# Performance work log

Hardware: AMD Instinct MI355X
Metric: run time of the kernel (lower is better)

## Reference

```python
import jax, jax.numpy as jnp
import numpy as np

B, T, N = 16, 256, 20000
REGIONS, TOPK = 20000, 0.2
IN_DIM = int(REGIONS * TOPK ** 2)   # 800
K = int(REGIONS * TOPK)             # 4000
R = 1000                            # rest_limitation
ZCOLS = K + R                       # all-False mask columns per sample


def setup_inputs() -> dict:
    key = jax.random.key(0)
    ks = jax.random.split(key, 8)
    x = jax.random.normal(ks[0], (B, T, IN_DIM), jnp.float32)
    # first ZCOLS voxel columns are never covered (mask False), rest are covered
    border_mask = jnp.concatenate(
        [jnp.zeros((B, T, ZCOLS), bool), jnp.ones((B, T, N - ZCOLS), bool)], axis=-1)
    # K distinct indices per sample, drawn from the uncovered columns [0, ZCOLS)
    index = jax.vmap(lambda k: jax.random.permutation(k, ZCOLS)[:K])(
        jax.random.split(ks[1], B)).astype(jnp.int32)
    s1 = 1.0 / np.sqrt(IN_DIM); s2 = 1.0 / np.sqrt(K)
    W1 = jax.random.uniform(ks[2], (IN_DIM, K), jnp.float32, -s1, s1)
    b1 = jax.random.uniform(ks[3], (K,), jnp.float32, -s1, s1)
    W2 = jax.random.uniform(ks[4], (K, K), jnp.float32, -s2, s2)
    b2 = jax.random.uniform(ks[5], (K,), jnp.float32, -s2, s2)
    W3 = jax.random.uniform(ks[6], (K, R), jnp.float32, -s2, s2)
    b3 = jax.random.uniform(ks[7], (R,), jnp.float32, -s2, s2)
    return dict(x=x, border_mask=border_mask, index=index,
                W1=W1, b1=b1, W2=W2, b2=b2, W3=W3, b3=b3)


def reference(x, border_mask, index, W1, b1, W2, b2, W3, b3):
    h = x @ W1 + b1                  # unzip   [B,T,K]
    h = h @ W2 + b2                  # unprocess [B,T,K]
    x_rest = h @ W3 + b3             # rest    [B,T,R]
    colsum = border_mask.sum(axis=1)                 # [B,N] per-voxel coverage count
    idx_member = jax.vmap(lambda i: jnp.zeros((N,), bool).at[i].set(True))(index)
    # scatter h into indexed voxel columns
    x_recon = jax.vmap(lambda i, hb: jnp.zeros((T, N), h.dtype).at[:, i].set(hb))(index, h)
    # rest positions: uncovered columns not already taken by index (sorted order)
    rest_mask = (colsum == 0) & ~idx_member          # [B,N]
    rank = jnp.cumsum(rest_mask, axis=-1) - 1        # position among rest columns
    valid = rest_mask & (rank < R)                   # cap at rest_limitation ('adjust')
    g = jnp.take_along_axis(
        x_rest, jnp.broadcast_to(jnp.clip(rank, 0, R - 1)[:, None, :], (B, T, N)), axis=-1)
    return jnp.where(valid[:, None, :], g, x_recon)
```

## Files before the change

### kernel.cpp

```cpp
#include <hip/hip_runtime.h>

typedef __attribute__((ext_vector_type(4))) float f32x4;
typedef __attribute__((ext_vector_type(8))) __bf16 bf16x8;

#define B_SZ   16
#define T_SZ   256
#define BT_SZ  4096
#define N_VOX  20000
#define INDIM  800
#define K1P    1024
#define K_DIM  4000
#define KP     4096
#define R_DIM  1000
#define RP     1024

__device__ __forceinline__ unsigned short f2bf(float f) {
  unsigned int u = __builtin_bit_cast(unsigned int, f);
  u += 0x7fffu + ((u >> 16) & 1u);
  return (unsigned short)(u >> 16);
}
__device__ __forceinline__ float bf2f(unsigned short h) {
  unsigned int u = ((unsigned int)h) << 16;
  return __builtin_bit_cast(float, u);
}
__device__ __forceinline__ void gload16(const void* g, void* l) {
  __builtin_amdgcn_global_load_lds(
      (const __attribute__((address_space(1))) void*)g,
      (__attribute__((address_space(3))) void*)l, 16, 0, 0);
}

__global__ void cvt_pad_x(const float* __restrict__ src,
                          unsigned short* __restrict__ dst) {
  int i = blockIdx.x * 256 + threadIdx.x;
  int row = i >> 8;
  int c4 = i & 255;
  if (row >= BT_SZ) return;
  ushort4 o = {0, 0, 0, 0};
  if (c4 < INDIM / 4) {
    float4 v = ((const float4*)(src + (size_t)row * INDIM))[c4];
    o.x = f2bf(v.x); o.y = f2bf(v.y); o.z = f2bf(v.z); o.w = f2bf(v.w);
  }
  ((ushort4*)(dst + (size_t)row * K1P))[c4] = o;
}

__global__ void transpose_cvt(const float* __restrict__ W,
                              unsigned short* __restrict__ WT,
                              int K, int N, int Kpad, int Npad) {
  __shared__ float tile[32][33];
  int k0 = blockIdx.x * 32, n0 = blockIdx.y * 32;
  for (int i = threadIdx.y; i < 32; i += 8) {
    int k = k0 + i, n = n0 + threadIdx.x;
    tile[i][threadIdx.x] = (k < K && n < N) ? W[(size_t)k * N + n] : 0.f;
  }
  __syncthreads();
  for (int i = threadIdx.y; i < 32; i += 8) {
    int n = n0 + i, k = k0 + threadIdx.x;
    if (n < Npad && k < Kpad)
      WT[(size_t)n * Kpad + k] = f2bf(tile[threadIdx.x][i]);
  }
}

__global__ void covered_kernel(const int* __restrict__ bmask,
                               unsigned char* __restrict__ cov) {
  int n4 = blockIdx.x * 256 + threadIdx.x;
  int b = blockIdx.y;
  if (n4 >= N_VOX / 4) return;
  const int4* p = (const int4*)(bmask + (size_t)b * T_SZ * N_VOX) + n4;
  int4 a = {0, 0, 0, 0};
  for (int t0 = 0; t0 < T_SZ; t0 += 8) {
    int4 c[8];
#pragma unroll
    for (int tt = 0; tt < 8; ++tt)
      c[tt] = p[(size_t)(t0 + tt) * (N_VOX / 4)];
#pragma unroll
    for (int tt = 0; tt < 8; ++tt) {
      a.x |= c[tt].x; a.y |= c[tt].y; a.z |= c[tt].z; a.w |= c[tt].w;
    }
    if (a.x && a.y && a.z && a.w) break;
  }
  uchar4 o;
  o.x = (unsigned char)(a.x != 0); o.y = (unsigned char)(a.y != 0);
  o.z = (unsigned char)(a.z != 0); o.w = (unsigned char)(a.w != 0);
  *(uchar4*)(cov + (size_t)b * N_VOX + (size_t)n4 * 4) = o;
}

__global__ void map_kernel(const int* __restrict__ index,
                           const unsigned char* __restrict__ cov,
                           int* __restrict__ srcmap) {
  int b = blockIdx.x, tid = threadIdx.x;
  int* sm = srcmap + (size_t)b * N_VOX;
  for (int n = tid; n < N_VOX; n += 1024) sm[n] = -1;
  __syncthreads();
  const int* idx = index + (size_t)b * K_DIM;
  for (int j = tid; j < K_DIM; j += 1024) sm[idx[j]] = j;
  __syncthreads();

  __shared__ int wsum[16];
  __shared__ int s_running;
  if (tid == 0) s_running = 0;
  __syncthreads();
  const int lane = tid & 63, wid = tid >> 6;
  const unsigned char* cv = cov + (size_t)b * N_VOX;
  for (int base = 0; base < N_VOX; base += 1024) {
    int n = base + tid;
    bool flag = (n < N_VOX) && (!cv[n]) && (sm[n] < 0);
    unsigned long long bal = __ballot(flag);
    if (lane == 0) wsum[wid] = __popcll(bal);
    __syncthreads();
    int woff = 0, tot = 0;
    for (int w = 0; w < 16; ++w) {
      int c = wsum[w];
      if (w < wid) woff += c;
      tot += c;
    }
    int rank = s_running + woff + __popcll(bal & ((1ull << lane) - 1ull));
    if (flag && rank < R_DIM) sm[n] = K_DIM + rank;
    __syncthreads();
    if (tid == 0) s_running += tot;
    __syncthreads();
  }
}

template <int BM>
__global__ __launch_bounds__(256) void gemm_bt(
    const unsigned short* __restrict__ A,
    const unsigned short* __restrict__ BTm,
    const float* __restrict__ bias, int nbias,
    unsigned short* __restrict__ C,
    int K, int lda, int ldb, int ldc) {
  constexpr int MI = BM / 32;
  __shared__ __align__(16) unsigned short As[BM * 32];
  __shared__ __align__(16) unsigned short Bs[128 * 32];
  const int tid = threadIdx.x;
  const int wid = tid >> 6;
  const int lane = tid & 63;
  const int bm = blockIdx.y, bn = blockIdx.x;
  const int wm = wid >> 1, wn = wid & 1;
  const int sub = lane >> 2;
  const int quad = lane & 3;

  const int rA0 = wid * 16 + sub;
  const char* gA0 = (const char*)(A + (size_t)(bm * BM + rA0) * lda) + quad * 16;
  const char* gA1 = (const char*)(A + (size_t)(bm * BM + ((BM == 128) ? rA0 + 64 : rA0)) * lda) + quad * 16;
  const char* gB0 = (const char*)(BTm + (size_t)(bn * 128 + rA0) * ldb) + quad * 16;
  const char* gB1 = (const char*)(BTm + (size_t)(bn * 128 + rA0 + 64) * ldb) + quad * 16;

  char* lA0 = (char*)As + wid * 1024 + lane * 16;
  char* lA1 = lA0 + 4096;
  char* lB0 = (char*)Bs + wid * 1024 + lane * 16;
  char* lB1 = lB0 + 4096;

  const int r15 = lane & 15;
  const int kg = lane >> 4;

  f32x4 acc[MI][4] = {};

  for (int kt = 0; kt < K; kt += 32) {
    const int kb = kt * 2;
    gload16(gA0 + kb, lA0);
    if constexpr (BM == 128) gload16(gA1 + kb, lA1);
    gload16(gB0 + kb, lB0);
    gload16(gB1 + kb, lB1);
    __syncthreads();
    bf16x8 af[MI], bfr[4];
#pragma unroll
    for (int i = 0; i < MI; ++i)
      af[i] = *(const bf16x8*)&As[(wm * (BM / 2) + i * 16 + r15) * 32 + kg * 8];
#pragma unroll
    for (int j = 0; j < 4; ++j)
      bfr[j] = *(const bf16x8*)&Bs[(wn * 64 + j * 16 + r15) * 32 + kg * 8];
#pragma unroll
    for (int i = 0; i < MI; ++i)
#pragma unroll
      for (int j = 0; j < 4; ++j)
        acc[i][j] = __builtin_amdgcn_mfma_f32_16x16x32_bf16(af[i], bfr[j], acc[i][j], 0, 0, 0);
    __syncthreads();
  }

#pragma unroll
  for (int i = 0; i < MI; ++i) {
    const int row0 = bm * BM + wm * (BM / 2) + i * 16 + kg * 4;
#pragma unroll
    for (int j = 0; j < 4; ++j) {
      const int col = bn * 128 + wn * 64 + j * 16 + r15;
      const float bv = bias[(col < nbias) ? col : (nbias - 1)];
#pragma unroll
      for (int r = 0; r < 4; ++r)
        C[(size_t)(row0 + r) * ldc + col] = f2bf(acc[i][j][r] + bv);
    }
  }
}

__global__ __launch_bounds__(512, 2) void gemm256(
    const unsigned short* __restrict__ A,
    const unsigned short* __restrict__ BTm,
    const float* __restrict__ bias, int nbias,
    unsigned short* __restrict__ C,
    int K, int lda, int ldb, int ldc) {
  __shared__ __align__(16) char smem[131072];
  const int tid = threadIdx.x;
  const int wid = tid >> 6, lane = tid & 63;
  const int wm = wid >> 2, wn = wid & 3;
  const int r15 = lane & 15, kg = lane >> 4;
  const int bm = blockIdx.y, bn = blockIdx.x;

  const int srow = tid >> 2;
  const int scol = (tid & 3) * 8;
  const unsigned short* gA = A + (size_t)(bm * 256 + srow) * lda + scol;
  const unsigned short* gB = BTm + (size_t)(bn * 256 + srow) * ldb + scol;

  const int aoff = (wm * 128 + r15) * 64 + kg * 16;
  const int boff = (wn * 64 + r15) * 64 + kg * 16;

  f32x4 acc[8][4] = {};
  bf16x8 bfr[4];

#define STAGE_HALF(S, MAT, KH, TN)                                            \
  {                                                                           \
    const unsigned short* g =                                                 \
        ((MAT) ? gB : gA) + (size_t)(TN) * 64 + (KH) * 32;                    \
    char* l = smem + (S) * 65536 + (MAT) * 32768 + (KH) * 16384 + tid * 16;   \
    gload16(g, l);                                                            \
    gload16(g + (size_t)128 * ((MAT) ? ldb : lda), l + 8192);                 \
  }

#define PHASE(S, KS, MH, TN, DOVM)                                            \
  {                                                                           \
    bf16x8 af[4];                                                             \
    if ((MH) == 0) {                                                          \
      _Pragma("unroll")                                                       \
      for (int j = 0; j < 4; ++j)                                             \
        bfr[j] = *(const bf16x8*)(smem + (S) * 65536 + 32768 +                \
                                  (KS) * 16384 + boff + j * 1024);            \
    }                                                                         \
    _Pragma("unroll")                                                         \
    for (int i = 0; i < 4; ++i)                                               \
      af[i] = *(const bf16x8*)(smem + (S) * 65536 + (KS) * 16384 +            \
                               (MH) * 4096 + aoff + i * 1024);                \
    STAGE_HALF((S) ^ 1, (MH), (KS), TN)                                       \
    if (DOVM) asm volatile("s_waitcnt vmcnt(4)" ::: "memory");                \
    asm volatile("s_barrier" ::: "memory");                                   \
    __builtin_amdgcn_s_setprio(1);                                            \
    _Pragma("unroll")                                                         \
    for (int i = 0; i < 4; ++i)                                               \
      _Pragma("unroll")                                                       \
      for (int j = 0; j < 4; ++j)                                             \
        acc[(MH) * 4 + i][j] = __builtin_amdgcn_mfma_f32_16x16x32_bf16(       \
            af[i], bfr[j], acc[(MH) * 4 + i][j], 0, 0, 0);                    \
    __builtin_amdgcn_s_setprio(0);                                            \
    asm volatile("s_barrier" ::: "memory");                                   \
  }

#define TILE4(S, TN)                                                          \
  PHASE(S, 0, 0, TN, 0)                                                       \
  PHASE(S, 0, 1, TN, 1)                                                       \
  PHASE(S, 1, 0, TN, 0)                                                       \
  PHASE(S, 1, 1, TN, 1)

  const int NT = K >> 6;
  STAGE_HALF(0, 0, 0, 0)
  STAGE_HALF(0, 1, 0, 0)
  STAGE_HALF(0, 0, 1, 0)
  STAGE_HALF(0, 1, 1, 0)
  asm volatile("s_waitcnt vmcnt(4)" ::: "memory");
  asm volatile("s_barrier" ::: "memory");

  for (int tp = 0; tp < NT; tp += 2) {
    const int tn1 = tp + 1;
    TILE4(0, tn1)
    const int tn2 = (tp + 2 < NT) ? tp + 2 : NT - 1;
    TILE4(1, tn2)
  }

#undef STAGE_HALF
#undef PHASE
#undef TILE4

#pragma unroll
  for (int f = 0; f < 8; ++f) {
    const int row0 = bm * 256 + wm * 128 + f * 16 + kg * 4;
#pragma unroll
    for (int j = 0; j < 4; ++j) {
      const int col = bn * 256 + wn * 64 + j * 16 + r15;
      const float bv = bias[(col < nbias) ? col : (nbias - 1)];
#pragma unroll
      for (int r = 0; r < 4; ++r)
        C[(size_t)(row0 + r) * ldc + col] = f2bf(acc[f][j][r] + bv);
    }
  }
}

__global__ void fill_out(const int* __restrict__ srcmap,
                         const unsigned short* __restrict__ h2b,
                         const unsigned short* __restrict__ xrb,
                         float* __restrict__ out) {
  int n4 = blockIdx.x * 256 + threadIdx.x;
  if (n4 >= N_VOX / 4) return;
  int t = blockIdx.y, b = blockIdx.z;
  size_t bt = (size_t)b * T_SZ + t;
  const int4 sm = ((const int4*)(srcmap + (size_t)b * N_VOX))[n4];
  const unsigned short* hrow = h2b + bt * KP;
  const unsigned short* xrow = xrb + bt * RP;
  float4 v;
  v.x = (sm.x < 0) ? 0.f : bf2f(sm.x < K_DIM ? hrow[sm.x] : xrow[sm.x - K_DIM]);
  v.y = (sm.y < 0) ? 0.f : bf2f(sm.y < K_DIM ? hrow[sm.y] : xrow[sm.y - K_DIM]);
  v.z = (sm.z < 0) ? 0.f : bf2f(sm.z < K_DIM ? hrow[sm.z] : xrow[sm.z - K_DIM]);
  v.w = (sm.w < 0) ? 0.f : bf2f(sm.w < K_DIM ? hrow[sm.w] : xrow[sm.w - K_DIM]);
  ((float4*)(out + bt * N_VOX))[n4] = v;
}

extern "C" void kernel_launch(void* const* d_in, const int* in_sizes, int n_in,
                              void* d_out, int out_size, void* d_ws, size_t ws_size,
                              hipStream_t stream) {
  const float* x          = (const float*)d_in[0];
  const int* bm           = (const int*)d_in[1];
  const int* index        = (const int*)d_in[2];
  const float* W1         = (const float*)d_in[3];
  const float* b1         = (const float*)d_in[4];
  const float* W2         = (const float*)d_in[5];
  const float* b2         = (const float*)d_in[6];
  const float* W3         = (const float*)d_in[7];
  const float* b3         = (const float*)d_in[8];
  float* out = (float*)d_out;

  char* ws = (char*)d_ws;
  size_t off = 0;
  auto alloc = [&](size_t bytes) -> void* {
    void* p = ws + off;
    off += (bytes + 255) & ~(size_t)255;
    return p;
  };
  unsigned short* xb  = (unsigned short*)alloc((size_t)BT_SZ * K1P * 2);
  unsigned short* w1t = (unsigned short*)alloc((size_t)KP * K1P * 2);
  unsigned short* w2t = (unsigned short*)alloc((size_t)KP * KP * 2);
  unsigned short* w3t = (unsigned short*)alloc((size_t)RP * KP * 2);
  unsigned short* h1b = (unsigned short*)alloc((size_t)BT_SZ * KP * 2);
  unsigned short* h2b = (unsigned short*)alloc((size_t)BT_SZ * KP * 2);
  unsigned short* xrb = (unsigned short*)alloc((size_t)BT_SZ * RP * 2);
  unsigned char* cov = (unsigned char*)alloc((size_t)B_SZ * N_VOX);
  int* srcmap = (int*)alloc((size_t)B_SZ * N_VOX * 4);

  cvt_pad_x<<<BT_SZ * (K1P / 4) / 256, 256, 0, stream>>>(x, xb);
  {
    dim3 g(K1P / 32, KP / 32);
    transpose_cvt<<<g, dim3(32, 8), 0, stream>>>(W1, w1t, INDIM, K_DIM, K1P, KP);
  }
  {
    dim3 g(KP / 32, KP / 32);
    transpose_cvt<<<g, dim3(32, 8), 0, stream>>>(W2, w2t, K_DIM, K_DIM, KP, KP);
  }
  {
    dim3 g(KP / 32, RP / 32);
    transpose_cvt<<<g, dim3(32, 8), 0, stream>>>(W3, w3t, K_DIM, R_DIM, KP, RP);
  }

  {
    dim3 g((N_VOX / 4 + 255) / 256, B_SZ);
    covered_kernel<<<g, 256, 0, stream>>>(bm, cov);
  }
  map_kernel<<<B_SZ, 1024, 0, stream>>>(index, cov, srcmap);

  {
    dim3 g(KP / 256, BT_SZ / 256);
    gemm256<<<g, 512, 0, stream>>>(xb, w1t, b1, K_DIM, h1b, K1P, K1P, K1P, KP);
  }
  {
    dim3 g(KP / 256, BT_SZ / 256);
    gemm256<<<g, 512, 0, stream>>>(h1b, w2t, b2, K_DIM, h2b, KP, KP, KP, KP);
  }
  {
    dim3 g(RP / 128, BT_SZ / 64);
    gemm_bt<64><<<g, 256, 0, stream>>>(h2b, w3t, b3, R_DIM, xrb, KP, KP, KP, RP);
  }

  {
    dim3 g((N_VOX / 4 + 255) / 256, T_SZ, B_SZ);
    fill_out<<<g, 256, 0, stream>>>(srcmap, h2b, xrb, out);
  }
}
```

Measured before the change: 487.8 us.

## Split-K third GEMM, swizzle LDS in gemm256, trim K padding, nontemporal output stores

The third GEMM now uses 128-row tiles with a 4-way K split that writes bf16 partials, followed by a new reduce kernel that adds the bias. The first GEMM's K padding shrinks from 1024 to 896, cutting wasted MFMA work. gemm256 gains an XOR swizzle on LDS writes and reads to avoid bank conflicts, and fill_out uses nontemporal stores for the large output. Rounding each split-K partial to bf16 adds extra rounding error and extra memory traffic. The 896 pad must also divide cleanly into gemm256's K stepping.

```diff
diff --git a/kernel.cpp b/kernel.cpp
--- a/kernel.cpp
+++ b/kernel.cpp
@@ -8,11 +8,12 @@
 #define BT_SZ  4096
 #define N_VOX  20000
 #define INDIM  800
-#define K1P    1024
+#define K1P    896
 #define K_DIM  4000
 #define KP     4096
 #define R_DIM  1000
 #define RP     1024
+#define SPLITK 4
 
 __device__ __forceinline__ unsigned short f2bf(float f) {
   unsigned int u = __builtin_bit_cast(unsigned int, f);
@@ -31,10 +32,9 @@
 
 __global__ void cvt_pad_x(const float* __restrict__ src,
                           unsigned short* __restrict__ dst) {
-  int i = blockIdx.x * 256 + threadIdx.x;
-  int row = i >> 8;
-  int c4 = i & 255;
-  if (row >= BT_SZ) return;
+  int row = blockIdx.x;
+  int c4 = threadIdx.x;
+  if (c4 >= K1P / 4) return;
   ushort4 o = {0, 0, 0, 0};
   if (c4 < INDIM / 4) {
     float4 v = ((const float4*)(src + (size_t)row * INDIM))[c4];
@@ -121,13 +121,13 @@
   }
 }
 
-template <int BM>
+template <int BM, bool SPLIT>
 __global__ __launch_bounds__(256) void gemm_bt(
     const unsigned short* __restrict__ A,
     const unsigned short* __restrict__ BTm,
     const float* __restrict__ bias, int nbias,
     unsigned short* __restrict__ C,
-    int K, int lda, int ldb, int ldc) {
+    int K, int lda, int ldb, int ldc, size_t zstride) {
   constexpr int MI = BM / 32;
   __shared__ __align__(16) unsigned short As[BM * 32];
   __shared__ __align__(16) unsigned short Bs[128 * 32];
@@ -135,6 +135,12 @@
   const int wid = tid >> 6;
   const int lane = tid & 63;
   const int bm = blockIdx.y, bn = blockIdx.x;
+  if (SPLIT) {
+    int kz = blockIdx.z;
+    A += (size_t)kz * K;
+    BTm += (size_t)kz * K;
+    C += (size_t)kz * zstride;
+  }
   const int wm = wid >> 1, wn = wid & 1;
   const int sub = lane >> 2;
   const int quad = lane & 3;
@@ -183,12 +189,34 @@
 #pragma unroll
     for (int j = 0; j < 4; ++j) {
       const int col = bn * 128 + wn * 64 + j * 16 + r15;
-      const float bv = bias[(col < nbias) ? col : (nbias - 1)];
+      float bv = 0.f;
+      if constexpr (!SPLIT) bv = bias[(col < nbias) ? col : (nbias - 1)];
 #pragma unroll
       for (int r = 0; r < 4; ++r)
         C[(size_t)(row0 + r) * ldc + col] = f2bf(acc[i][j][r] + bv);
     }
   }
+}
+
+__global__ void reduce_splitk(const unsigned short* __restrict__ part,
+                              const float* __restrict__ bias,
+                              unsigned short* __restrict__ out) {
+  int i = blockIdx.x * 256 + threadIdx.x;
+  if (i >= BT_SZ * RP / 4) return;
+  const size_t zs = (size_t)BT_SZ * RP / 4;
+  float s[4] = {0.f, 0.f, 0.f, 0.f};
+#pragma unroll
+  for (int z = 0; z < SPLITK; ++z) {
+    ushort4 p = ((const ushort4*)part)[z * zs + i];
+    s[0] += bf2f(p.x); s[1] += bf2f(p.y); s[2] += bf2f(p.z); s[3] += bf2f(p.w);
+  }
+  int col = (i * 4) & (RP - 1);
+  ushort4 o;
+  o.x = f2bf(s[0] + bias[(col     < R_DIM) ? col     : R_DIM - 1]);
+  o.y = f2bf(s[1] + bias[(col + 1 < R_DIM) ? col + 1 : R_DIM - 1]);
+  o.z = f2bf(s[2] + bias[(col + 2 < R_DIM) ? col + 2 : R_DIM - 1]);
+  o.w = f2bf(s[3] + bias[(col + 3 < R_DIM) ? col + 3 : R_DIM - 1]);
+  ((ushort4*)out)[i] = o;
 }
 
 __global__ __launch_bounds__(512, 2) void gemm256(
@@ -205,12 +233,13 @@
   const int bm = blockIdx.y, bn = blockIdx.x;
 
   const int srow = tid >> 2;
-  const int scol = (tid & 3) * 8;
+  const int scol = ((tid & 3) * 8) ^ ((srow & 8) ? 16 : 0);
   const unsigned short* gA = A + (size_t)(bm * 256 + srow) * lda + scol;
   const unsigned short* gB = BTm + (size_t)(bn * 256 + srow) * ldb + scol;
 
-  const int aoff = (wm * 128 + r15) * 64 + kg * 16;
-  const int boff = (wn * 64 + r15) * 64 + kg * 16;
+  const int cxor = (kg * 16) ^ ((r15 & 8) ? 32 : 0);
+  const int aoff = (wm * 128 + r15) * 64 + cxor;
+  const int boff = (wn * 64 + r15) * 64 + cxor;
 
   f32x4 acc[8][4] = {};
   bf16x8 bfr[4];
@@ -301,12 +330,12 @@
   const int4 sm = ((const int4*)(srcmap + (size_t)b * N_VOX))[n4];
   const unsigned short* hrow = h2b + bt * KP;
   const unsigned short* xrow = xrb + bt * RP;
-  float4 v;
+  f32x4 v;
   v.x = (sm.x < 0) ? 0.f : bf2f(sm.x < K_DIM ? hrow[sm.x] : xrow[sm.x - K_DIM]);
   v.y = (sm.y < 0) ? 0.f : bf2f(sm.y < K_DIM ? hrow[sm.y] : xrow[sm.y - K_DIM]);
   v.z = (sm.z < 0) ? 0.f : bf2f(sm.z < K_DIM ? hrow[sm.z] : xrow[sm.z - K_DIM]);
   v.w = (sm.w < 0) ? 0.f : bf2f(sm.w < K_DIM ? hrow[sm.w] : xrow[sm.w - K_DIM]);
-  ((float4*)(out + bt * N_VOX))[n4] = v;
+  __builtin_nontemporal_store(v, (f32x4*)(out + bt * N_VOX) + n4);
 }
 
 extern "C" void kernel_launch(void* const* d_in, const int* in_sizes, int n_in,
@@ -330,17 +359,18 @@
     off += (bytes + 255) & ~(size_t)255;
     return p;
   };
-  unsigned short* xb  = (unsigned short*)alloc((size_t)BT_SZ * K1P * 2);
-  unsigned short* w1t = (unsigned short*)alloc((size_t)KP * K1P * 2);
-  unsigned short* w2t = (unsigned short*)alloc((size_t)KP * KP * 2);
-  unsigned short* w3t = (unsigned short*)alloc((size_t)RP * KP * 2);
-  unsigned short* h1b = (unsigned short*)alloc((size_t)BT_SZ * KP * 2);
-  unsigned short* h2b = (unsigned short*)alloc((size_t)BT_SZ * KP * 2);
-  unsigned short* xrb = (unsigned short*)alloc((size_t)BT_SZ * RP * 2);
+  unsigned short* xb   = (unsigned short*)alloc((size_t)BT_SZ * K1P * 2);
+  unsigned short* w1t  = (unsigned short*)alloc((size_t)KP * K1P * 2);
+  unsigned short* w2t  = (unsigned short*)alloc((size_t)KP * KP * 2);
+  unsigned short* w3t  = (unsigned short*)alloc((size_t)RP * KP * 2);
+  unsigned short* h1b  = (unsigned short*)alloc((size_t)BT_SZ * KP * 2);
+  unsigned short* h2b  = (unsigned short*)alloc((size_t)BT_SZ * KP * 2);
+  unsigned short* xrb  = (unsigned short*)alloc((size_t)BT_SZ * RP * 2);
+  unsigned short* xpart = (unsigned short*)alloc((size_t)SPLITK * BT_SZ * RP * 2);
   unsigned char* cov = (unsigned char*)alloc((size_t)B_SZ * N_VOX);
   int* srcmap = (int*)alloc((size_t)B_SZ * N_VOX * 4);
 
-  cvt_pad_x<<<BT_SZ * (K1P / 4) / 256, 256, 0, stream>>>(x, xb);
+  cvt_pad_x<<<BT_SZ, 256, 0, stream>>>(x, xb);
   {
     dim3 g(K1P / 32, KP / 32);
     transpose_cvt<<<g, dim3(32, 8), 0, stream>>>(W1, w1t, INDIM, K_DIM, K1P, KP);
@@ -369,9 +399,12 @@
     gemm256<<<g, 512, 0, stream>>>(h1b, w2t, b2, K_DIM, h2b, KP, KP, KP, KP);
   }
   {
-    dim3 g(RP / 128, BT_SZ / 64);
-    gemm_bt<64><<<g, 256, 0, stream>>>(h2b, w3t, b3, R_DIM, xrb, KP, KP, KP, RP);
-  }
+    dim3 g(RP / 128, BT_SZ / 128, SPLITK);
+    gemm_bt<128, true><<<g, 256, 0, stream>>>(h2b, w3t, nullptr, 0, xpart,
+                                              KP / SPLITK, KP, KP, RP,
+                                              (size_t)BT_SZ * RP);
+  }
+  reduce_splitk<<<(BT_SZ * RP / 4 + 255) / 256, 256, 0, stream>>>(xpart, b3, xrb);
 
   {
     dim3 g((N_VOX / 4 + 255) / 256, T_SZ, B_SZ);
```

New measurement: 433.1 us. 11.2% less time.
